# Optimization experiments

Hardware: AMD Instinct MI355X
Metric: run time of the kernel (lower is better)

The kernel has to match this reference:

```python
import jax, jax.numpy as jnp
import numpy as np

DT = 0.001
HIDDEN = 512
OUT = 128

def setup_inputs() -> dict:
    key = jax.random.key(0)
    k1, k2 = jax.random.split(key)
    x = jax.random.normal(k1, (64, 2048, HIDDEN), dtype=jnp.float32)
    # torch Linear default init ~ U(-1/sqrt(fan_in), 1/sqrt(fan_in)), weight shape [out, in]
    lim = 1.0 / np.sqrt(HIDDEN)
    W = jax.random.uniform(k2, (OUT, HIDDEN), dtype=jnp.float32, minval=-lim, maxval=lim)
    tau_syn = jnp.asarray(0.5, dtype=jnp.float32)  # tau_syn_out (used as tau_syn_inv)
    tau_mem = jnp.asarray(0.5, dtype=jnp.float32)  # tau_mem_out (used as tau_mem_inv)
    return {"x": x, "W": W, "tau_syn": tau_syn, "tau_mem": tau_mem}

def reference(x, W, tau_syn, tau_mem):
    # SNNDecode.forward: clamp taus, permute to [seq, batch, in], per-step
    # Linear + norse LI (leaky integrator) feed-forward step with v_leak = 0.
    tau_syn = jnp.clip(tau_syn, 0.0, 1.0)
    tau_mem = jnp.clip(tau_mem, 0.0, 1.0)
    batch, seq, _ = x.shape
    # The per-step Linear is recurrence-independent: hoist it into one big GEMM.
    # z_all: [seq, batch, out]
    z_all = jnp.einsum('bsh,oh->sbo', x, W)
    v0 = jnp.zeros((batch, OUT), dtype=x.dtype)
    i0 = jnp.zeros((batch, OUT), dtype=x.dtype)

    def step(carry, z):
        v, i = carry
        # li_feed_forward_step: dv = dt*tau_mem_inv*((v_leak - v) + i)
        v_new = v + DT * tau_mem * (i - v)
        i_dec = i - DT * tau_syn * i
        i_new = i_dec + z
        return (v_new, i_new), v_new

    (v_f, i_f), voltages = jax.lax.scan(step, (v0, i0), z_all)
    # output stacked over time: [seq, batch, out]; final state (v, i)
    return voltages, v_f, i_f
```

## Files before the change

### kernel.cpp

```cpp
#include <hip/hip_runtime.h>
#include <hip/hip_bf16.h>


typedef __attribute__((ext_vector_type(4))) float    f4;
typedef __attribute__((ext_vector_type(8))) short    s8;
typedef __attribute__((ext_vector_type(4))) unsigned u4;

#define SEQ    2048
#define HID    512
#define CHAINS 8192
#define VOLT   16777216
#define NCH    64
#define CHUNK  32

__device__ __forceinline__ float clamp01(float x) { return fminf(fmaxf(x, 0.f), 1.f); }

__device__ __forceinline__ unsigned pkbf(float x, float y) {
  float2 t; t.x = x; t.y = y;
  union { __hip_bfloat162 h; unsigned u; } c;
  c.h = __float22bfloat162_rn(t);
  return c.u;
}

__device__ __forceinline__ short f2bf(float f) {
  union { float f; unsigned u; } c; c.f = f;
  unsigned u = c.u;
  unsigned r = (u + 0x7fffu + ((u >> 16) & 1u)) >> 16;
  return (short)r;
}

__device__ __forceinline__ int swz(int row, int k) {
  return (row * 64 + k) ^ ((row & 7) << 3);
}

__global__ __launch_bounds__(256) void k_wconv(const float* __restrict__ W,
                                               unsigned short* __restrict__ Wb) {
  const int i = blockIdx.x * 256 + threadIdx.x;
  const f4 lo = ((const f4*)W)[2 * i];
  const f4 hi = ((const f4*)W)[2 * i + 1];
  s8 v;
#pragma unroll
  for (int j = 0; j < 4; ++j) { v[j] = f2bf(lo[j]); v[j + 4] = f2bf(hi[j]); }
  ((s8*)Wb)[i] = v;
}

__global__ __launch_bounds__(256, 2) void k_gemm(const float* __restrict__ X,
                                                 const unsigned short* __restrict__ Wb,
                                                 float* __restrict__ Z,
                                                 const float* __restrict__ tau_syn,
                                                 const float* __restrict__ tau_mem,
                                                 float* __restrict__ ws) {
  __shared__ __align__(16) char smem[65536];
  short* const AS = (short*)smem;
  float* const ZS = (float*)smem;

  const int tid = threadIdx.x;
  const int blk = blockIdx.x;
  const int m0  = blk << 7;
  const int bI  = blk >> 4;
  const int t0  = (blk & 15) << 7;

  const int rbase = tid >> 3;
  const int coff  = (tid & 7) << 3;

  const int lane = tid & 63;
  const int wid  = tid >> 6;
  const int wmb  = (wid >> 1) << 6;
  const int wnb  = (wid & 1) << 6;
  const int lr   = lane & 15;
  const int lk   = (lane >> 4) << 3;

  const float* pX[4];
#pragma unroll
  for (int c = 0; c < 4; ++c)
    pX[c] = X + (size_t)(m0 + (c << 5) + rbase) * HID + coff;
  const unsigned short* pB[4];
#pragma unroll
  for (int ni = 0; ni < 4; ++ni)
    pB[ni] = Wb + (size_t)(wnb + (ni << 4) + lr) * HID + lk;

  f4 acc[4][4];
#pragma unroll
  for (int mi = 0; mi < 4; ++mi)
#pragma unroll
    for (int ni = 0; ni < 4; ++ni) acc[mi][ni] = (f4){0.f, 0.f, 0.f, 0.f};

  f4 xa[3][4][2];
#pragma unroll
  for (int c = 0; c < 4; ++c) {
    xa[0][c][0] = *(const f4*)(pX[c]);
    xa[0][c][1] = *(const f4*)(pX[c] + 4);
    xa[1][c][0] = *(const f4*)(pX[c] + 64);
    xa[1][c][1] = *(const f4*)(pX[c] + 68);
  }

#pragma unroll
  for (int ks = 0; ks < 8; ++ks) {
    const int cur = ks % 3;
    short* const Ac = AS + ((ks & 1) << 13);
#pragma unroll
    for (int c = 0; c < 4; ++c) {
      const int row = (c << 5) + rbase;
      u4 va;
      va[0] = pkbf(xa[cur][c][0][0], xa[cur][c][0][1]);
      va[1] = pkbf(xa[cur][c][0][2], xa[cur][c][0][3]);
      va[2] = pkbf(xa[cur][c][1][0], xa[cur][c][1][1]);
      va[3] = pkbf(xa[cur][c][1][2], xa[cur][c][1][3]);
      *(u4*)&Ac[swz(row, coff)] = va;
    }
    __syncthreads();
    s8 bg[2][4];
#pragma unroll
    for (int kk = 0; kk < 2; ++kk)
#pragma unroll
      for (int ni = 0; ni < 4; ++ni)
        bg[kk][ni] = *(const s8*)(pB[ni] + (ks << 6) + (kk << 5));
    if (ks < 6) {
      const int k0 = (ks + 2) << 6;
      const int nxt = (ks + 2) % 3;
#pragma unroll
      for (int c = 0; c < 4; ++c) {
        xa[nxt][c][0] = *(const f4*)(pX[c] + k0);
        xa[nxt][c][1] = *(const f4*)(pX[c] + k0 + 4);
      }
    }
#pragma unroll
    for (int kk = 0; kk < 2; ++kk) {
      s8 af[4];
#pragma unroll
      for (int mi = 0; mi < 4; ++mi)
        af[mi] = *(const s8*)&Ac[swz(wmb + (mi << 4) + lr, (kk << 5) + lk)];
#pragma unroll
      for (int mi = 0; mi < 4; ++mi)
#pragma unroll
        for (int ni = 0; ni < 4; ++ni)
          acc[mi][ni] = __builtin_amdgcn_mfma_f32_16x16x32_bf16(af[mi], bg[kk][ni],
                                                                acc[mi][ni], 0, 0, 0);
    }
  }

  __syncthreads();
  const int rr = (lane >> 4) << 2;
#pragma unroll
  for (int mi = 0; mi < 4; ++mi)
#pragma unroll
    for (int ni = 0; ni < 4; ++ni)
#pragma unroll
      for (int r = 0; r < 4; ++r)
        ZS[(wmb + (mi << 4) + rr + r) * 128 + wnb + (ni << 4) + lr] = acc[mi][ni][r];
  __syncthreads();

  {
    float* const Zrow = Z + (size_t)t0 * 8192 + (bI << 7);
#pragma unroll
    for (int i = 0; i < 16; ++i) {
      const int idx  = (i << 8) + tid;
      const int toff = idx >> 5;
      const int c4   = idx & 31;
      *(f4*)(Zrow + (size_t)toff * 8192 + (c4 << 2)) = *(const f4*)&ZS[toff * 128 + (c4 << 2)];
    }
  }
  {
    const float a  = 0.001f * clamp01(tau_mem[0]);
    const float eb = 1.f - 0.001f * clamp01(tau_syn[0]);
    const int col = tid & 127, h = tid >> 7;
    const int chain = (bI << 7) + col;
#pragma unroll
    for (int s = 0; s < 2; ++s) {
      const int r0 = (h << 6) + (s << 5);
      const float* zs = ZS + r0 * 128 + col;
      float v = 0.f, ii = 0.f;
#pragma unroll 8
      for (int j = 0; j < CHUNK; ++j) {
        const float z = zs[j * 128];
        v  = v + a * (ii - v);
        ii = eb * ii + z;
      }
      const int q = ((blk & 15) << 2) + (h << 1) + s;
      ws[q * CHAINS + chain]                 = v;
      ws[NCH * CHAINS + q * CHAINS + chain]  = ii;
    }
  }
}

__global__ __launch_bounds__(256) void k_emit(const float* __restrict__ tau_syn,
                                              const float* __restrict__ tau_mem,
                                              float* Z,
                                              const float* __restrict__ ws) {
  const int tid = threadIdx.x;
  const int cg = (blockIdx.x & 31) * 64 + (tid & 63);
  const int q  = (blockIdx.x >> 5) * 4 + (tid >> 6);
  const float a  = 0.001f * clamp01(tau_mem[0]);
  const float bb = 0.001f * clamp01(tau_syn[0]);
  const float ea = 1.f - a, eb = 1.f - bb;
  float P = 1.f, Q = 0.f, R = 1.f;
#pragma unroll
  for (int j = 0; j < CHUNK; ++j) { float Pn = P * ea; Q = P * a + Q * eb; P = Pn; R *= eb; }

  const f4* vend = (const f4*)ws;
  const f4* iend = vend + NCH * 2048;
  f4 sv = (f4){0.f, 0.f, 0.f, 0.f}, si = (f4){0.f, 0.f, 0.f, 0.f};
#pragma unroll 4
  for (int p = 0; p < q; ++p) {
    const f4 ve = vend[p * 2048 + cg];
    const f4 ie = iend[p * 2048 + cg];
    const f4 nv = P * sv + Q * si + ve;
    si = R * si + ie;
    sv = nv;
  }

  f4* z4 = (f4*)Z;
  const int tb = q << 5;
  f4 v = sv, ii = si;
#pragma unroll 8
  for (int j = 0; j < CHUNK; ++j) {
    const size_t idx = (size_t)(tb + j) * 2048 + cg;
    f4 z = z4[idx];
    v  = v + a * (ii - v);
    z4[idx] = v;
    ii = eb * ii + z;
  }
  if (q == NCH - 1) {
    ((f4*)(Z + VOLT))[cg]        = v;
    ((f4*)(Z + VOLT + CHAINS))[cg] = ii;
  }
}

extern "C" void kernel_launch(void* const* d_in, const int* in_sizes, int n_in,
                              void* d_out, int out_size, void* d_ws, size_t ws_size,
                              hipStream_t stream) {
  const float* X   = (const float*)d_in[0];
  const float* W   = (const float*)d_in[1];
  const float* tsy = (const float*)d_in[2];
  const float* tme = (const float*)d_in[3];
  float* Out = (float*)d_out;
  float* ws  = (float*)d_ws;
  unsigned short* Wb = (unsigned short*)((char*)d_ws + (4u << 20));

  k_wconv<<<32, 256, 0, stream>>>(W, Wb);
  k_gemm<<<1024, 256, 0, stream>>>(X, Wb, Out, tsy, tme, ws);
  k_emit<<<512, 256, 0, stream>>>(tsy, tme, Out, ws);
}
```

Before: 104.8 us.

## Fuse GEMM and chunked scan into one persistent kernel with grid barrier

Merges the GEMM and emit kernels into a single kernel of 512 blocks. Each block computes two 128-step tiles, runs the local scan in shared memory, publishes tile end states, then waits on a global atomic barrier before applying the carry-in correction. The second tile stays resident in LDS and is written once, so it avoids being stored to global memory and then read and rewritten by a second pass. The first tile is still re-read and updated in global memory. This relies on all 512 blocks being co-resident for the spin barrier, which risks deadlock if occupancy is lower, and it adds a memset and the barrier wait.

Result: slower. 361.7 us (+245.2%).

```diff
diff --git a/kernel.cpp b/kernel.cpp
--- a/kernel.cpp
+++ b/kernel.cpp
@@ -10,8 +10,8 @@
 #define HID    512
 #define CHAINS 8192
 #define VOLT   16777216
-#define NCH    64
-#define CHUNK  32
+#define NT     16
+#define NBLK   512
 
 __device__ __forceinline__ float clamp01(float x) { return fminf(fmaxf(x, 0.f), 1.f); }
 
@@ -44,185 +44,253 @@
   ((s8*)Wb)[i] = v;
 }
 
-__global__ __launch_bounds__(256, 2) void k_gemm(const float* __restrict__ X,
+__global__ __launch_bounds__(256, 2) void k_main(const float* __restrict__ X,
                                                  const unsigned short* __restrict__ Wb,
-                                                 float* __restrict__ Z,
+                                                 float* __restrict__ Out,
                                                  const float* __restrict__ tau_syn,
                                                  const float* __restrict__ tau_mem,
-                                                 float* __restrict__ ws) {
+                                                 float* __restrict__ ws,
+                                                 unsigned* __restrict__ ctr) {
   __shared__ __align__(16) char smem[65536];
+  __shared__ __align__(16) float tAs[128], tBs[128];
+  __shared__ __align__(16) float vh[2][128], ih[2][128];
+  __shared__ __align__(16) float inV[2][128], inI[2][128];
+  __shared__ float sc[2];
   short* const AS = (short*)smem;
   float* const ZS = (float*)smem;
 
   const int tid = threadIdx.x;
   const int blk = blockIdx.x;
-  const int m0  = blk << 7;
-  const int bI  = blk >> 4;
-  const int t0  = (blk & 15) << 7;
+  const int r   = blk >> 3;
+  const int k   = blk & 7;
+
+  const float a  = 0.001f * clamp01(tau_mem[0]);
+  const float bb = 0.001f * clamp01(tau_syn[0]);
+  const float ea = 1.f - a, eb = 1.f - bb;
+
+  if (tid == 0) {
+    float al = 1.f, be = 0.f, ep = 1.f;
+    for (int j = 0; j < 128; ++j) {
+      const float aln = al * ea;
+      be = al * a + be * eb;
+      al = aln;
+      ep *= eb;
+      tAs[j] = al; tBs[j] = be;
+      if (j == 63) sc[0] = ep;
+    }
+    sc[1] = ep;
+  }
 
   const int rbase = tid >> 3;
   const int coff  = (tid & 7) << 3;
-
-  const int lane = tid & 63;
-  const int wid  = tid >> 6;
-  const int wmb  = (wid >> 1) << 6;
-  const int wnb  = (wid & 1) << 6;
-  const int lr   = lane & 15;
-  const int lk   = (lane >> 4) << 3;
-
-  const float* pX[4];
-#pragma unroll
-  for (int c = 0; c < 4; ++c)
-    pX[c] = X + (size_t)(m0 + (c << 5) + rbase) * HID + coff;
+  const int lane  = tid & 63;
+  const int wid   = tid >> 6;
+  const int wmb   = (wid >> 1) << 6;
+  const int wnb   = (wid & 1) << 6;
+  const int lr    = lane & 15;
+  const int lk    = (lane >> 4) << 3;
+
   const unsigned short* pB[4];
 #pragma unroll
   for (int ni = 0; ni < 4; ++ni)
     pB[ni] = Wb + (size_t)(wnb + (ni << 4) + lr) * HID + lk;
 
-  f4 acc[4][4];
-#pragma unroll
-  for (int mi = 0; mi < 4; ++mi)
-#pragma unroll
-    for (int ni = 0; ni < 4; ++ni) acc[mi][ni] = (f4){0.f, 0.f, 0.f, 0.f};
-
-  f4 xa[3][4][2];
-#pragma unroll
-  for (int c = 0; c < 4; ++c) {
-    xa[0][c][0] = *(const f4*)(pX[c]);
-    xa[0][c][1] = *(const f4*)(pX[c] + 4);
-    xa[1][c][0] = *(const f4*)(pX[c] + 64);
-    xa[1][c][1] = *(const f4*)(pX[c] + 68);
-  }
-
-#pragma unroll
-  for (int ks = 0; ks < 8; ++ks) {
-    const int cur = ks % 3;
-    short* const Ac = AS + ((ks & 1) << 13);
+  for (int tile = 0; tile < 2; ++tile) {
+    const int jt = (k << 1) + tile;
+    const int m0 = (r << 11) + (jt << 7);
+    __syncthreads();
+
+    const float* pX[4];
+#pragma unroll
+    for (int c = 0; c < 4; ++c)
+      pX[c] = X + (size_t)(m0 + (c << 5) + rbase) * HID + coff;
+
+    f4 acc[4][4];
+#pragma unroll
+    for (int mi = 0; mi < 4; ++mi)
+#pragma unroll
+      for (int ni = 0; ni < 4; ++ni) acc[mi][ni] = (f4){0.f, 0.f, 0.f, 0.f};
+
+    f4 xa[3][4][2];
 #pragma unroll
     for (int c = 0; c < 4; ++c) {
-      const int row = (c << 5) + rbase;
-      u4 va;
-      va[0] = pkbf(xa[cur][c][0][0], xa[cur][c][0][1]);
-      va[1] = pkbf(xa[cur][c][0][2], xa[cur][c][0][3]);
-      va[2] = pkbf(xa[cur][c][1][0], xa[cur][c][1][1]);
-      va[3] = pkbf(xa[cur][c][1][2], xa[cur][c][1][3]);
-      *(u4*)&Ac[swz(row, coff)] = va;
-    }
+      xa[0][c][0] = *(const f4*)(pX[c]);
+      xa[0][c][1] = *(const f4*)(pX[c] + 4);
+      xa[1][c][0] = *(const f4*)(pX[c] + 64);
+      xa[1][c][1] = *(const f4*)(pX[c] + 68);
+    }
+
+#pragma unroll
+    for (int ks = 0; ks < 8; ++ks) {
+      const int cur = ks % 3;
+      short* const Ac = AS + ((ks & 1) << 13);
+#pragma unroll
+      for (int c = 0; c < 4; ++c) {
+        const int row = (c << 5) + rbase;
+        u4 va;
+        va[0] = pkbf(xa[cur][c][0][0], xa[cur][c][0][1]);
+        va[1] = pkbf(xa[cur][c][0][2], xa[cur][c][0][3]);
+        va[2] = pkbf(xa[cur][c][1][0], xa[cur][c][1][1]);
+        va[3] = pkbf(xa[cur][c][1][2], xa[cur][c][1][3]);
+        *(u4*)&Ac[swz(row, coff)] = va;
+      }
+      __syncthreads();
+      s8 bg[2][4];
+#pragma unroll
+      for (int kk = 0; kk < 2; ++kk)
+#pragma unroll
+        for (int ni = 0; ni < 4; ++ni)
+          bg[kk][ni] = *(const s8*)(pB[ni] + (ks << 6) + (kk << 5));
+      if (ks < 6) {
+        const int k0 = (ks + 2) << 6;
+        const int nxt = (ks + 2) % 3;
+#pragma unroll
+        for (int c = 0; c < 4; ++c) {
+          xa[nxt][c][0] = *(const f4*)(pX[c] + k0);
+          xa[nxt][c][1] = *(const f4*)(pX[c] + k0 + 4);
+        }
+      }
+#pragma unroll
+      for (int kk = 0; kk < 2; ++kk) {
+        s8 af[4];
+#pragma unroll
+        for (int mi = 0; mi < 4; ++mi)
+          af[mi] = *(const s8*)&Ac[swz(wmb + (mi << 4) + lr, (kk << 5) + lk)];
+#pragma unroll
+        for (int mi = 0; mi < 4; ++mi)
+#pragma unroll
+          for (int ni = 0; ni < 4; ++ni)
+            acc[mi][ni] = __builtin_amdgcn_mfma_f32_16x16x32_bf16(af[mi], bg[kk][ni],
+                                                                  acc[mi][ni], 0, 0, 0);
+      }
+    }
+
     __syncthreads();
-    s8 bg[2][4];
-#pragma unroll
-    for (int kk = 0; kk < 2; ++kk)
+    const int rr = (lane >> 4) << 2;
+#pragma unroll
+    for (int mi = 0; mi < 4; ++mi)
 #pragma unroll
       for (int ni = 0; ni < 4; ++ni)
-        bg[kk][ni] = *(const s8*)(pB[ni] + (ks << 6) + (kk << 5));
-    if (ks < 6) {
-      const int k0 = (ks + 2) << 6;
-      const int nxt = (ks + 2) % 3;
-#pragma unroll
-      for (int c = 0; c < 4; ++c) {
-        xa[nxt][c][0] = *(const f4*)(pX[c] + k0);
-        xa[nxt][c][1] = *(const f4*)(pX[c] + k0 + 4);
-      }
-    }
-#pragma unroll
-    for (int kk = 0; kk < 2; ++kk) {
-      s8 af[4];
-#pragma unroll
-      for (int mi = 0; mi < 4; ++mi)
-        af[mi] = *(const s8*)&Ac[swz(wmb + (mi << 4) + lr, (kk << 5) + lk)];
-#pragma unroll
-      for (int mi = 0; mi < 4; ++mi)
-#pragma unroll
-        for (int ni = 0; ni < 4; ++ni)
-          acc[mi][ni] = __builtin_amdgcn_mfma_f32_16x16x32_bf16(af[mi], bg[kk][ni],
-                                                                acc[mi][ni], 0, 0, 0);
-    }
-  }
-
+#pragma unroll
+        for (int rg = 0; rg < 4; ++rg)
+          ZS[(wmb + (mi << 4) + rr + rg) * 128 + wnb + (ni << 4) + lr] = acc[mi][ni][rg];
+    __syncthreads();
+
+    {
+      const int h = tid >> 7, col = tid & 127;
+      float* zc = ZS + ((h << 6) * 128) + col;
+      float v = 0.f, ii = 0.f;
+#pragma unroll 8
+      for (int j = 0; j < 64; ++j) {
+        const float z = zc[j * 128];
+        v  = v + a * (ii - v);
+        zc[j * 128] = v;
+        ii = eb * ii + z;
+      }
+      vh[h][col] = v; ih[h][col] = ii;
+    }
+    __syncthreads();
+    {
+      const int col = tid & 127, jh = tid >> 7;
+      const float v0 = vh[0][col], i0 = ih[0][col];
+      float* zc1 = ZS + (64 + (jh << 5)) * 128 + col;
+#pragma unroll 8
+      for (int jj = 0; jj < 32; ++jj) {
+        const int j = (jh << 5) + jj;
+        zc1[jj * 128] += tAs[j] * v0 + tBs[j] * i0;
+      }
+    }
+    if (tid < 128) {
+      const int col = tid;
+      const float vE = vh[1][col] + tAs[63] * vh[0][col] + tBs[63] * ih[0][col];
+      const float iE = ih[1][col] + sc[0] * ih[0][col];
+      ws[(size_t)jt * CHAINS + (r << 7) + col]        = vE;
+      ws[(size_t)(NT + jt) * CHAINS + (r << 7) + col] = iE;
+    }
+    if (tile == 0) {
+      __syncthreads();
+      float* const Orow = Out + (size_t)(jt << 7) * 8192 + (r << 7);
+#pragma unroll
+      for (int i = 0; i < 16; ++i) {
+        const int idx  = (i << 8) + tid;
+        const int toff = idx >> 5;
+        const int c4   = idx & 31;
+        *(f4*)(Orow + (size_t)toff * 8192 + (c4 << 2)) = *(const f4*)&ZS[toff * 128 + (c4 << 2)];
+      }
+    }
+  }
+
+  __threadfence();
   __syncthreads();
-  const int rr = (lane >> 4) << 2;
-#pragma unroll
-  for (int mi = 0; mi < 4; ++mi)
-#pragma unroll
-    for (int ni = 0; ni < 4; ++ni)
-#pragma unroll
-      for (int r = 0; r < 4; ++r)
-        ZS[(wmb + (mi << 4) + rr + r) * 128 + wnb + (ni << 4) + lr] = acc[mi][ni][r];
+  if (tid == 0) {
+    __hip_atomic_fetch_add(ctr, 1u, __ATOMIC_RELEASE, __HIP_MEMORY_SCOPE_AGENT);
+    while (__hip_atomic_load(ctr, __ATOMIC_ACQUIRE, __HIP_MEMORY_SCOPE_AGENT) < NBLK)
+      __builtin_amdgcn_s_sleep(8);
+  }
   __syncthreads();
+  __threadfence();
+
+  const int jtA = k << 1, jtB = jtA + 1;
+  const float P = tAs[127], Q = tBs[127], R = sc[1];
+  if (tid < 128) {
+    const int col = tid, chain = (r << 7) + col;
+    float sv = 0.f, si = 0.f;
+    for (int p = 0; p < jtA; ++p) {
+      const float ve = ws[(size_t)p * CHAINS + chain];
+      const float ie = ws[(size_t)(NT + p) * CHAINS + chain];
+      const float nv = P * sv + Q * si + ve;
+      si = R * si + ie;
+      sv = nv;
+    }
+    inV[0][col] = sv; inI[0][col] = si;
+    const float eAv = ws[(size_t)jtA * CHAINS + chain];
+    const float eAi = ws[(size_t)(NT + jtA) * CHAINS + chain];
+    const float bv2 = P * sv + Q * si + eAv;
+    const float bi2 = R * si + eAi;
+    inV[1][col] = bv2; inI[1][col] = bi2;
+    if (k == 7) {
+      const float eBv = ws[(size_t)jtB * CHAINS + chain];
+      const float eBi = ws[(size_t)(NT + jtB) * CHAINS + chain];
+      Out[VOLT + chain]          = P * bv2 + Q * bi2 + eBv;
+      Out[VOLT + CHAINS + chain] = R * bi2 + eBi;
+    }
+  }
+  __syncthreads();
 
   {
-    float* const Zrow = Z + (size_t)t0 * 8192 + (bI << 7);
+    const int col = tid & 127, jh = tid >> 7;
+    const float bv = inV[1][col], bi = inI[1][col];
+    float* zc = ZS + ((jh << 6) * 128) + col;
+#pragma unroll 8
+    for (int jj = 0; jj < 64; ++jj) {
+      const int j = (jh << 6) + jj;
+      zc[jj * 128] += tAs[j] * bv + tBs[j] * bi;
+    }
+  }
+  __syncthreads();
+
+  {
+    float* const OrowB = Out + (size_t)(jtB << 7) * 8192 + (r << 7);
 #pragma unroll
     for (int i = 0; i < 16; ++i) {
       const int idx  = (i << 8) + tid;
       const int toff = idx >> 5;
       const int c4   = idx & 31;
-      *(f4*)(Zrow + (size_t)toff * 8192 + (c4 << 2)) = *(const f4*)&ZS[toff * 128 + (c4 << 2)];
+      *(f4*)(OrowB + (size_t)toff * 8192 + (c4 << 2)) = *(const f4*)&ZS[toff * 128 + (c4 << 2)];
     }
   }
   {
-    const float a  = 0.001f * clamp01(tau_mem[0]);
-    const float eb = 1.f - 0.001f * clamp01(tau_syn[0]);
-    const int col = tid & 127, h = tid >> 7;
-    const int chain = (bI << 7) + col;
-#pragma unroll
-    for (int s = 0; s < 2; ++s) {
-      const int r0 = (h << 6) + (s << 5);
-      const float* zs = ZS + r0 * 128 + col;
-      float v = 0.f, ii = 0.f;
-#pragma unroll 8
-      for (int j = 0; j < CHUNK; ++j) {
-        const float z = zs[j * 128];
-        v  = v + a * (ii - v);
-        ii = eb * ii + z;
-      }
-      const int q = ((blk & 15) << 2) + (h << 1) + s;
-      ws[q * CHAINS + chain]                 = v;
-      ws[NCH * CHAINS + q * CHAINS + chain]  = ii;
-    }
-  }
-}
-
-__global__ __launch_bounds__(256) void k_emit(const float* __restrict__ tau_syn,
-                                              const float* __restrict__ tau_mem,
-                                              float* Z,
-                                              const float* __restrict__ ws) {
-  const int tid = threadIdx.x;
-  const int cg = (blockIdx.x & 31) * 64 + (tid & 63);
-  const int q  = (blockIdx.x >> 5) * 4 + (tid >> 6);
-  const float a  = 0.001f * clamp01(tau_mem[0]);
-  const float bb = 0.001f * clamp01(tau_syn[0]);
-  const float ea = 1.f - a, eb = 1.f - bb;
-  float P = 1.f, Q = 0.f, R = 1.f;
-#pragma unroll
-  for (int j = 0; j < CHUNK; ++j) { float Pn = P * ea; Q = P * a + Q * eb; P = Pn; R *= eb; }
-
-  const f4* vend = (const f4*)ws;
-  const f4* iend = vend + NCH * 2048;
-  f4 sv = (f4){0.f, 0.f, 0.f, 0.f}, si = (f4){0.f, 0.f, 0.f, 0.f};
-#pragma unroll 4
-  for (int p = 0; p < q; ++p) {
-    const f4 ve = vend[p * 2048 + cg];
-    const f4 ie = iend[p * 2048 + cg];
-    const f4 nv = P * sv + Q * si + ve;
-    si = R * si + ie;
-    sv = nv;
-  }
-
-  f4* z4 = (f4*)Z;
-  const int tb = q << 5;
-  f4 v = sv, ii = si;
-#pragma unroll 8
-  for (int j = 0; j < CHUNK; ++j) {
-    const size_t idx = (size_t)(tb + j) * 2048 + cg;
-    f4 z = z4[idx];
-    v  = v + a * (ii - v);
-    z4[idx] = v;
-    ii = eb * ii + z;
-  }
-  if (q == NCH - 1) {
-    ((f4*)(Z + VOLT))[cg]        = v;
-    ((f4*)(Z + VOLT + CHAINS))[cg] = ii;
+    float* const OrowA = Out + (size_t)(jtA << 7) * 8192 + (r << 7);
+#pragma unroll
+    for (int i = 0; i < 16; ++i) {
+      const int idx  = (i << 8) + tid;
+      const int toff = idx >> 5;
+      const int c4   = idx & 31;
+      f4* p = (f4*)(OrowA + (size_t)toff * 8192 + (c4 << 2));
+      const f4 vv = *(const f4*)&inV[0][c4 << 2];
+      const f4 iv = *(const f4*)&inI[0][c4 << 2];
+      *p = *p + tAs[toff] * vv + tBs[toff] * iv;
+    }
   }
 }
 
@@ -235,9 +303,10 @@
   const float* tme = (const float*)d_in[3];
   float* Out = (float*)d_out;
   float* ws  = (float*)d_ws;
-  unsigned short* Wb = (unsigned short*)((char*)d_ws + (4u << 20));
-
+  unsigned short* Wb = (unsigned short*)((char*)d_ws + (1u << 20));
+  unsigned* ctr = (unsigned*)((char*)d_ws + (1u << 20) + (128u << 10));
+
+  hipMemsetAsync(ctr, 0, 4, stream);
   k_wconv<<<32, 256, 0, stream>>>(W, Wb);
-  k_gemm<<<1024, 256, 0, stream>>>(X, Wb, Out, tsy, tme, ws);
-  k_emit<<<512, 256, 0, stream>>>(tsy, tme, Out, ws);
-}
+  k_main<<<NBLK, 256, 0, stream>>>(X, Wb, Out, tsy, tme, ws, ctr);
+}
```
